# Performance work log

Measured on AMD Instinct MI355X. Metric: run time of the kernel, lower is better.

Reference implementation:

```python
import jax, jax.numpy as jnp
import numpy as np

B, N, D = 2, 2048, 768
HEADS, DIM_HEAD = 12, 64
INNER = HEADS * DIM_HEAD  # 768
OUT_DIM = 768


def setup_inputs() -> dict:
    key = jax.random.key(0)
    k1, k2, k3, k4, k5 = jax.random.split(key, 5)
    s_in = 1.0 / np.sqrt(D)
    s_inner = 1.0 / np.sqrt(INNER)
    return {
        "x": jax.random.normal(k1, (B, N, D), dtype=jnp.float32),
        "w_qkv": jax.random.normal(k2, (D, 3 * INNER), dtype=jnp.float32) * s_in,
        "b_qkv": jax.random.normal(k3, (3 * INNER,), dtype=jnp.float32) * 0.01,
        "w_out": jax.random.normal(k4, (INNER, OUT_DIM), dtype=jnp.float32) * s_inner,
        "b_out": jax.random.normal(k5, (OUT_DIM,), dtype=jnp.float32) * 0.01,
    }


def reference(x, w_qkv, b_qkv, w_out, b_out):
    b, n, _ = x.shape
    scale = DIM_HEAD ** -0.5
    qkv = x @ w_qkv + b_qkv                      # [b, n, 3*inner]
    q, k, v = jnp.split(qkv, 3, axis=-1)
    # 'b n (h d) -> b h n d'
    reshape = lambda t: t.reshape(b, n, HEADS, DIM_HEAD).transpose(0, 2, 1, 3)
    q, k, v = reshape(q), reshape(k), reshape(v)
    dots = jnp.einsum("bhnd,bhmd->bhnm", q, k) * scale
    attn = jax.nn.softmax(dots, axis=-1)
    out = jnp.einsum("bhnm,bhmd->bhnd", attn, v)  # [b, h, n, d]
    out = out.transpose(0, 2, 1, 3).reshape(b, n, INNER)
    return out @ w_out + b_out
```

## Files before the change

### kernel.cpp

```cpp
#include <hip/hip_runtime.h>
#include <hip/hip_bf16.h>
#include <stdint.h>


typedef __attribute__((ext_vector_type(8))) short bf16x8;
typedef __attribute__((ext_vector_type(4))) float f32x4;
typedef __attribute__((address_space(3))) unsigned int lds_uint;
typedef __attribute__((address_space(1))) const unsigned int g_uint;

__device__ __forceinline__ short f2bf(float f) {
    union { float f; uint32_t u; } x; x.f = f;
    uint32_t r = (x.u + 0x7fffu + ((x.u >> 16) & 1u)) >> 16;
    return (short)r;
}
__device__ __forceinline__ uint32_t packbf(float a, float b) {
    union { float f; uint32_t u; } xa, xb; xa.f = a; xb.f = b;
    return __builtin_amdgcn_perm(xb.u + 0x8000u, xa.u + 0x8000u, 0x07060302u);
}
__device__ __forceinline__ float exp2fast(float x) {
#if __has_builtin(__builtin_amdgcn_exp2f)
    return __builtin_amdgcn_exp2f(x);
#else
    return __expf(x * 0.6931471805599453f);
#endif
}
__device__ __forceinline__ void gl_lds16(const void* g, void* l) {
    __builtin_amdgcn_global_load_lds((g_uint*)g, (lds_uint*)l, 16, 0, 0);
}

__device__ __forceinline__ void tr_tile(const float* __restrict__ W,
                                        short* __restrict__ Wt, int K, int N,
                                        int n0, int k0, int t, short* S) {
    {
        int kl = t >> 2, ng = t & 3;
        const float* src = W + (size_t)(k0 + kl) * N + n0 + ng * 16;
        #pragma unroll
        for (int j = 0; j < 16; j += 4) {
            float4 f = *(const float4*)(src + j);
            S[(ng*16 + j + 0) * 65 + kl] = f2bf(f.x);
            S[(ng*16 + j + 1) * 65 + kl] = f2bf(f.y);
            S[(ng*16 + j + 2) * 65 + kl] = f2bf(f.z);
            S[(ng*16 + j + 3) * 65 + kl] = f2bf(f.w);
        }
    }
    __syncthreads();
    {
        int nl = t >> 2, kg = t & 3;
        short* dst = Wt + (size_t)(n0 + nl) * K + k0 + kg * 16;
        #pragma unroll
        for (int j = 0; j < 16; j += 4) {
            short4 s4;
            s4.x = S[nl*65 + kg*16 + j + 0];
            s4.y = S[nl*65 + kg*16 + j + 1];
            s4.z = S[nl*65 + kg*16 + j + 2];
            s4.w = S[nl*65 + kg*16 + j + 3];
            *(short4*)(dst + j) = s4;
        }
    }
}

__global__ __launch_bounds__(256)
void prep_k(const float* __restrict__ x, short* __restrict__ Xb,
            const float* __restrict__ Wq, short* __restrict__ Wqt,
            const float* __restrict__ Wo, short* __restrict__ Wot)
{
    __shared__ short S[64 * 65];
    const int t = threadIdx.x;
    if (blockIdx.x < 1536) {
        int i = (blockIdx.x * 256 + t) * 8;
        float4 f0 = *(const float4*)(x + i);
        float4 f1 = *(const float4*)(x + i + 4);
        short s[8];
        s[0]=f2bf(f0.x); s[1]=f2bf(f0.y); s[2]=f2bf(f0.z); s[3]=f2bf(f0.w);
        s[4]=f2bf(f1.x); s[5]=f2bf(f1.y); s[6]=f2bf(f1.z); s[7]=f2bf(f1.w);
        *(uint4*)(Xb + i) = *(uint4*)s;
        return;
    }
    if (blockIdx.x < 1968) {
        const int b2 = blockIdx.x - 1536;
        tr_tile(Wq, Wqt, 768, 2304, (b2 % 36) * 64, (b2 / 36) * 64, t, S);
    } else {
        const int b3 = blockIdx.x - 1968;
        tr_tile(Wo, Wot, 768, 768, (b3 % 12) * 64, (b3 / 12) * 64, t, S);
    }
}

__global__ __launch_bounds__(256)
void tr_w(const float* __restrict__ W, short* __restrict__ Wt, int K, int N) {
    __shared__ short S[64 * 65];
    tr_tile(W, Wt, K, N, blockIdx.x * 64, blockIdx.y * 64, threadIdx.x, S);
}

__global__ __launch_bounds__(256)
void gemm_qkv(const short* __restrict__ A, const short* __restrict__ Bt,
              const float* __restrict__ bias,
              short* __restrict__ Qb, short* __restrict__ Kb, short* __restrict__ Vt)
{
    __shared__ short As[2][128 * 32];
    __shared__ short Bs[2][96 * 32];
    const int tid = threadIdx.x, lane = tid & 63, w = tid >> 6;
    const int wm = w >> 1, wn = w & 1, quad = lane >> 4, lcol = lane & 15;
    const int bm = blockIdx.y * 128, bn = blockIdx.x * 96;

    f32x4 acc[4][3];
    #pragma unroll
    for (int i = 0; i < 4; i++)
        #pragma unroll
        for (int j = 0; j < 3; j++) acc[i][j] = (f32x4){0.f, 0.f, 0.f, 0.f};

    {
        #pragma unroll
        for (int i = 0; i < 2; i++) {
            int c = tid + i * 256, row = c >> 2, cs = c & 3;
            gl_lds16(A + (size_t)(bm + row) * 768 + cs * 8, As[0] + c * 8);
        }
        int c = tid, row = c >> 2, cs = c & 3;
        gl_lds16(Bt + (size_t)(bn + row) * 768 + cs * 8, Bs[0] + c * 8);
        if (tid < 128) {
            int c2 = 256 + tid, row2 = c2 >> 2, cs2 = c2 & 3;
            gl_lds16(Bt + (size_t)(bn + row2) * 768 + cs2 * 8, Bs[0] + c2 * 8);
        }
    }
    __syncthreads();

    for (int it = 0; it < 24; it++) {
        const int p = it & 1;
        if (it < 23) {
            int kt = (it + 1) * 32;
            #pragma unroll
            for (int i = 0; i < 2; i++) {
                int c = tid + i * 256, row = c >> 2, cs = c & 3;
                gl_lds16(A + (size_t)(bm + row) * 768 + kt + cs * 8, As[p ^ 1] + c * 8);
            }
            int c = tid, row = c >> 2, cs = c & 3;
            gl_lds16(Bt + (size_t)(bn + row) * 768 + kt + cs * 8, Bs[p ^ 1] + c * 8);
            if (tid < 128) {
                int c2 = 256 + tid, row2 = c2 >> 2, cs2 = c2 & 3;
                gl_lds16(Bt + (size_t)(bn + row2) * 768 + kt + cs2 * 8, Bs[p ^ 1] + c2 * 8);
            }
        }
        bf16x8 a[4], b[3];
        #pragma unroll
        for (int tm = 0; tm < 4; tm++)
            a[tm] = *(const bf16x8*)(As[p] + (wm*64 + tm*16 + lcol) * 32 + quad * 8);
        #pragma unroll
        for (int tn = 0; tn < 3; tn++)
            b[tn] = *(const bf16x8*)(Bs[p] + (wn*48 + tn*16 + lcol) * 32 + quad * 8);
        #pragma unroll
        for (int tm = 0; tm < 4; tm++)
            #pragma unroll
            for (int tn = 0; tn < 3; tn++)
                acc[tm][tn] = __builtin_amdgcn_mfma_f32_16x16x32_bf16(a[tm], b[tn], acc[tm][tn], 0, 0, 0);
        __syncthreads();
    }

    const float SCLQ = 0.18033688011112042f;
    #pragma unroll
    for (int tm = 0; tm < 4; tm++) {
        #pragma unroll
        for (int tn = 0; tn < 3; tn++) {
            int col = bn + wn*48 + tn*16 + lcol;
            float bv = bias[col];
            int which = (col >= 1536) ? 2 : (col >= 768 ? 1 : 0);
            int cc = col - which * 768;
            int h = cc >> 6, d = cc & 63;
            int rowbase = bm + wm*64 + tm*16 + quad*4;
            int bb = rowbase >> 11, n0 = rowbase & 2047;
            int bh = bb * 12 + h;
            if (which == 2) {
                short4 s4;
                s4.x = f2bf(acc[tm][tn][0] + bv);
                s4.y = f2bf(acc[tm][tn][1] + bv);
                s4.z = f2bf(acc[tm][tn][2] + bv);
                s4.w = f2bf(acc[tm][tn][3] + bv);
                *(short4*)(Vt + (((size_t)bh*32 + (n0 >> 6))*64 + d)*64 + (n0 & 63)) = s4;
            } else {
                #pragma unroll
                for (int reg = 0; reg < 4; reg++) {
                    float v = acc[tm][tn][reg] + bv;
                    if (which == 0) v *= SCLQ;
                    short* dst = (which == 0) ? Qb : Kb;
                    dst[((size_t)bh*2048 + n0 + reg)*64 + d] = f2bf(v);
                }
            }
        }
    }
}

__global__ __launch_bounds__(256)
void attn_k(const short* __restrict__ Q, const short* __restrict__ K,
            const short* __restrict__ Vt, short* __restrict__ Ab)
{
    __shared__ short Ks[2][4096];
    __shared__ short Vs[2][4096];
    __shared__ short Ps[64 * 72];
    __shared__ float lsum[64];

    const int tid = threadIdx.x, lane = tid & 63, w = tid >> 6;
    const int quad = lane >> 4, lcol = lane & 15;
    const int bid = blockIdx.x;
    const int bh = bid % 24, qt = bid / 24;
    const int b = bh / 12, h = bh - b * 12;

    const short* Kg = K  + (size_t)bh * 131072;
    const short* Vg = Vt + (size_t)bh * 131072;

    bf16x8 qf[4][2];
    {
        const short* Qg = Q + ((size_t)bh * 2048 + (size_t)qt * 64) * 64;
        #pragma unroll
        for (int qs = 0; qs < 4; qs++)
            #pragma unroll
            for (int ks = 0; ks < 2; ks++)
                qf[qs][ks] = *(const bf16x8*)(Qg + (qs*16 + lcol) * 64 + ks*32 + quad*8);
    }

    if (tid < 64) lsum[tid] = 0.f;
    #pragma unroll
    for (int i = 0; i < 2; i++) {
        int c = tid + i * 256, row = c >> 3, cs = c & 7, gc = cs ^ (row & 7);
        gl_lds16(Kg + row * 64 + gc * 8, Ks[0] + c * 8);
        gl_lds16(Vg + row * 64 + gc * 8, Vs[0] + c * 8);
    }
    __syncthreads();

    f32x4 o[4];
    #pragma unroll
    for (int tn = 0; tn < 4; tn++) o[tn] = (f32x4){0.f, 0.f, 0.f, 0.f};
    float lp[4] = {0.f, 0.f, 0.f, 0.f};

    const int krow = w * 16 + lcol;
    const int ksw  = krow & 7;

    for (int kt = 0; kt < 32; kt++) {
        const int p = kt & 1;
        if (kt < 31) {
            #pragma unroll
            for (int i = 0; i < 2; i++) {
                int c = tid + i * 256, row = c >> 3, cs = c & 7, gc = cs ^ (row & 7);
                gl_lds16(Kg + (kt + 1) * 4096 + row * 64 + gc * 8, Ks[p ^ 1] + c * 8);
                gl_lds16(Vg + (kt + 1) * 4096 + row * 64 + gc * 8, Vs[p ^ 1] + c * 8);
            }
        }

        f32x4 st[4];
        #pragma unroll
        for (int qs = 0; qs < 4; qs++) st[qs] = (f32x4){0.f, 0.f, 0.f, 0.f};
        #pragma unroll
        for (int ks = 0; ks < 2; ks++) {
            bf16x8 kf = *(const bf16x8*)(Ks[p] + krow * 64 + (((ks*4 + quad) ^ ksw) << 3));
            #pragma unroll
            for (int qs = 0; qs < 4; qs++)
                st[qs] = __builtin_amdgcn_mfma_f32_16x16x32_bf16(kf, qf[qs][ks], st[qs], 0, 0, 0);
        }

        #pragma unroll
        for (int qs = 0; qs < 4; qs++) {
            float p0 = exp2fast(st[qs][0]), p1 = exp2fast(st[qs][1]);
            float p2 = exp2fast(st[qs][2]), p3 = exp2fast(st[qs][3]);
            lp[qs] += (p0 + p1) + (p2 + p3);
            uint32_t uu[2] = { packbf(p0, p1), packbf(p2, p3) };
            *(uint32_t*)(Ps + (qs*16 + lcol) * 72 + w*16 + quad*4)     = uu[0];
            *(uint32_t*)(Ps + (qs*16 + lcol) * 72 + w*16 + quad*4 + 2) = uu[1];
        }
        __syncthreads();

        #pragma unroll
        for (int ks = 0; ks < 2; ks++) {
            bf16x8 ap = *(const bf16x8*)(Ps + (w*16 + lcol) * 72 + ks * 32 + quad * 8);
            #pragma unroll
            for (int tn = 0; tn < 4; tn++) {
                int row = tn * 16 + lcol;
                bf16x8 bv = *(const bf16x8*)(Vs[p] + row * 64 +
                                             (((ks * 4 + quad) ^ (row & 7)) << 3));
                o[tn] = __builtin_amdgcn_mfma_f32_16x16x32_bf16(ap, bv, o[tn], 0, 0, 0);
            }
        }
        __syncthreads();
    }

    #pragma unroll
    for (int qs = 0; qs < 4; qs++) {
        float v = lp[qs];
        v += __shfl_xor(v, 16, 64);
        v += __shfl_xor(v, 32, 64);
        if (quad == 0) atomicAdd(&lsum[qs*16 + lcol], v);
    }
    __syncthreads();
    #pragma unroll
    for (int tn = 0; tn < 4; tn++) {
        #pragma unroll
        for (int r = 0; r < 4; r++) {
            int q = qt * 64 + w * 16 + quad * 4 + r;
            int d = h * 64 + tn * 16 + lcol;
            float rl = 1.0f / lsum[w * 16 + quad * 4 + r];
            Ab[((size_t)(b * 2048 + q)) * 768 + d] = f2bf(o[tn][r] * rl);
        }
    }
}

__global__ __launch_bounds__(256)
void gemm_out(const short* __restrict__ A, const short* __restrict__ Bt,
              const float* __restrict__ bias, float* __restrict__ Of)
{
    __shared__ short As[2][64 * 32];
    __shared__ short Bs[2][96 * 32];
    const int tid = threadIdx.x, lane = tid & 63, w = tid >> 6;
    const int wm = w >> 1, wn = w & 1, quad = lane >> 4, lcol = lane & 15;
    const int bm = blockIdx.y * 64, bn = blockIdx.x * 96;

    f32x4 acc[2][3];
    #pragma unroll
    for (int i = 0; i < 2; i++)
        #pragma unroll
        for (int j = 0; j < 3; j++) acc[i][j] = (f32x4){0.f, 0.f, 0.f, 0.f};

    {
        int row = tid >> 2, cs = tid & 3;
        gl_lds16(A  + (size_t)(bm + row) * 768 + cs * 8, As[0] + tid * 8);
        gl_lds16(Bt + (size_t)(bn + row) * 768 + cs * 8, Bs[0] + tid * 8);
        if (tid < 128) {
            int c = 256 + tid, row2 = c >> 2, cs2 = c & 3;
            gl_lds16(Bt + (size_t)(bn + row2) * 768 + cs2 * 8, Bs[0] + c * 8);
        }
    }
    __syncthreads();

    for (int it = 0; it < 24; it++) {
        const int p = it & 1;
        if (it < 23) {
            int kt = (it + 1) * 32;
            int row = tid >> 2, cs = tid & 3;
            gl_lds16(A  + (size_t)(bm + row) * 768 + kt + cs * 8, As[p ^ 1] + tid * 8);
            gl_lds16(Bt + (size_t)(bn + row) * 768 + kt + cs * 8, Bs[p ^ 1] + tid * 8);
            if (tid < 128) {
                int c = 256 + tid, row2 = c >> 2, cs2 = c & 3;
                gl_lds16(Bt + (size_t)(bn + row2) * 768 + kt + cs2 * 8, Bs[p ^ 1] + c * 8);
            }
        }
        bf16x8 a[2], b[3];
        #pragma unroll
        for (int tm = 0; tm < 2; tm++)
            a[tm] = *(const bf16x8*)(As[p] + (wm*32 + tm*16 + lcol) * 32 + quad * 8);
        #pragma unroll
        for (int tn = 0; tn < 3; tn++)
            b[tn] = *(const bf16x8*)(Bs[p] + (wn*48 + tn*16 + lcol) * 32 + quad * 8);
        #pragma unroll
        for (int tm = 0; tm < 2; tm++)
            #pragma unroll
            for (int tn = 0; tn < 3; tn++)
                acc[tm][tn] = __builtin_amdgcn_mfma_f32_16x16x32_bf16(a[tm], b[tn], acc[tm][tn], 0, 0, 0);
        __syncthreads();
    }
    #pragma unroll
    for (int tm = 0; tm < 2; tm++) {
        #pragma unroll
        for (int tn = 0; tn < 3; tn++) {
            int col = bn + wn*48 + tn*16 + lcol;
            float bv = bias[col];
            #pragma unroll
            for (int reg = 0; reg < 4; reg++) {
                int row = bm + wm*32 + tm*16 + quad*4 + reg;
                Of[(size_t)row * 768 + col] = acc[tm][tn][reg] + bv;
            }
        }
    }
}

extern "C" void kernel_launch(void* const* d_in, const int* in_sizes, int n_in,
                              void* d_out, int out_size, void* d_ws, size_t ws_size,
                              hipStream_t stream)
{
    (void)in_sizes; (void)n_in; (void)out_size;
    const float* x     = (const float*)d_in[0];
    const float* w_qkv = (const float*)d_in[1];
    const float* b_qkv = (const float*)d_in[2];
    const float* w_out = (const float*)d_in[3];
    const float* b_out = (const float*)d_in[4];
    float* out = (float*)d_out;

    const size_t XSZ = (size_t)4096 * 768;
    const size_t WQ  = (size_t)2304 * 768;
    const size_t WO  = (size_t)768 * 768;
    const size_t HSZ = (size_t)24 * 2048 * 64;
    short* Xb  = (short*)d_ws;
    short* Wqt = Xb + XSZ;
    short* Qb  = Wqt + WQ;
    short* Kb  = Qb + HSZ;
    short* Vt  = Kb + HSZ;
    short* Ab  = Xb;

    const bool sepWot = ws_size >= (XSZ + WQ + 3*HSZ + WO) * sizeof(short);
    short* Wot = sepWot ? (Vt + HSZ) : Wqt;

    if (sepWot) {
        prep_k<<<2112, 256, 0, stream>>>(x, Xb, w_qkv, Wqt, w_out, Wot);
        gemm_qkv<<<dim3(24, 32), 256, 0, stream>>>(Xb, Wqt, b_qkv, Qb, Kb, Vt);
    } else {
        prep_k<<<1968, 256, 0, stream>>>(x, Xb, w_qkv, Wqt, w_out, Wot);
        gemm_qkv<<<dim3(24, 32), 256, 0, stream>>>(Xb, Wqt, b_qkv, Qb, Kb, Vt);
        tr_w<<<dim3(12, 12), 256, 0, stream>>>(w_out, Wot, 768, 768);
    }
    attn_k<<<768, 256, 0, stream>>>(Qb, Kb, Vt, Ab);
    gemm_out<<<dim3(8, 64), 256, 0, stream>>>(Ab, Wot, b_out, out);
}
```

Measured before the change: 165.1 us.

## Keep attention probabilities in registers via permlane swap instead of LDS round-trip

The attention kernel now gives each wave its own 16 query rows across all 64 keys of a tile, instead of 16 keys across all 64 queries. The probabilities from the S=K·Q MFMA are packed to bf16 with v_cvt_pk_bf16_f32 and rearranged in registers with v_permlane16_swap. This replaces the shared-memory P buffer, its mid-loop __syncthreads, and the LDS atomic row-sum reduction with shuffles. The trade-off is more K-fragment LDS reads per wave, a remapped V column index to match the permuted operand layout, and gfx950-specific inline asm.

```diff
diff --git a/kernel.cpp b/kernel.cpp
--- a/kernel.cpp
+++ b/kernel.cpp
@@ -193,8 +193,6 @@
 {
     __shared__ short Ks[2][4096];
     __shared__ short Vs[2][4096];
-    __shared__ short Ps[64 * 72];
-    __shared__ float lsum[64];
 
     const int tid = threadIdx.x, lane = tid & 63, w = tid >> 6;
     const int quad = lane >> 4, lcol = lane & 15;
@@ -205,17 +203,14 @@
     const short* Kg = K  + (size_t)bh * 131072;
     const short* Vg = Vt + (size_t)bh * 131072;
 
-    bf16x8 qf[4][2];
+    bf16x8 qf[2];
     {
         const short* Qg = Q + ((size_t)bh * 2048 + (size_t)qt * 64) * 64;
         #pragma unroll
-        for (int qs = 0; qs < 4; qs++)
-            #pragma unroll
-            for (int ks = 0; ks < 2; ks++)
-                qf[qs][ks] = *(const bf16x8*)(Qg + (qs*16 + lcol) * 64 + ks*32 + quad*8);
-    }
-
-    if (tid < 64) lsum[tid] = 0.f;
+        for (int ks = 0; ks < 2; ks++)
+            qf[ks] = *(const bf16x8*)(Qg + (w*16 + lcol) * 64 + ks*32 + quad*8);
+    }
+
     #pragma unroll
     for (int i = 0; i < 2; i++) {
         int c = tid + i * 256, row = c >> 3, cs = c & 7, gc = cs ^ (row & 7);
@@ -227,10 +222,10 @@
     f32x4 o[4];
     #pragma unroll
     for (int tn = 0; tn < 4; tn++) o[tn] = (f32x4){0.f, 0.f, 0.f, 0.f};
-    float lp[4] = {0.f, 0.f, 0.f, 0.f};
-
-    const int krow = w * 16 + lcol;
-    const int ksw  = krow & 7;
+    float lp = 0.f;
+
+    const int ksw = lcol & 7;
+    const int bq  = ((quad & 1) << 1) | (quad >> 1);
 
     for (int kt = 0; kt < 32; kt++) {
         const int p = kt & 1;
@@ -245,56 +240,66 @@
 
         f32x4 st[4];
         #pragma unroll
-        for (int qs = 0; qs < 4; qs++) st[qs] = (f32x4){0.f, 0.f, 0.f, 0.f};
+        for (int kvs = 0; kvs < 4; kvs++) st[kvs] = (f32x4){0.f, 0.f, 0.f, 0.f};
         #pragma unroll
         for (int ks = 0; ks < 2; ks++) {
-            bf16x8 kf = *(const bf16x8*)(Ks[p] + krow * 64 + (((ks*4 + quad) ^ ksw) << 3));
-            #pragma unroll
-            for (int qs = 0; qs < 4; qs++)
-                st[qs] = __builtin_amdgcn_mfma_f32_16x16x32_bf16(kf, qf[qs][ks], st[qs], 0, 0, 0);
-        }
-
-        #pragma unroll
-        for (int qs = 0; qs < 4; qs++) {
-            float p0 = exp2fast(st[qs][0]), p1 = exp2fast(st[qs][1]);
-            float p2 = exp2fast(st[qs][2]), p3 = exp2fast(st[qs][3]);
-            lp[qs] += (p0 + p1) + (p2 + p3);
-            uint32_t uu[2] = { packbf(p0, p1), packbf(p2, p3) };
-            *(uint32_t*)(Ps + (qs*16 + lcol) * 72 + w*16 + quad*4)     = uu[0];
-            *(uint32_t*)(Ps + (qs*16 + lcol) * 72 + w*16 + quad*4 + 2) = uu[1];
-        }
-        __syncthreads();
-
+            #pragma unroll
+            for (int kvs = 0; kvs < 4; kvs++) {
+                bf16x8 kf = *(const bf16x8*)(Ks[p] + (kvs*16 + lcol) * 64 +
+                                             (((ks*4 + quad) ^ ksw) << 3));
+                st[kvs] = __builtin_amdgcn_mfma_f32_16x16x32_bf16(kf, qf[ks], st[kvs], 0, 0, 0);
+            }
+        }
+
+        uint32_t X[4], Y[4];
+        #pragma unroll
+        for (int kvs = 0; kvs < 4; kvs++) {
+            float p0 = exp2fast(st[kvs][0]), p1 = exp2fast(st[kvs][1]);
+            float p2 = exp2fast(st[kvs][2]), p3 = exp2fast(st[kvs][3]);
+            lp += (p0 + p1) + (p2 + p3);
+            asm("v_cvt_pk_bf16_f32 %0, %1, %2" : "=v"(X[kvs]) : "v"(p0), "v"(p1));
+            asm("v_cvt_pk_bf16_f32 %0, %1, %2" : "=v"(Y[kvs]) : "v"(p2), "v"(p3));
+        }
+
+        bf16x8 pa[2];
         #pragma unroll
         for (int ks = 0; ks < 2; ks++) {
-            bf16x8 ap = *(const bf16x8*)(Ps + (w*16 + lcol) * 72 + ks * 32 + quad * 8);
+            uint32_t a0 = X[2*ks], a1 = X[2*ks + 1];
+            uint32_t b0 = Y[2*ks], b1 = Y[2*ks + 1];
+            asm("v_permlane16_swap_b32 %0, %1" : "+v"(a0), "+v"(a1));
+            asm("v_permlane16_swap_b32 %0, %1" : "+v"(b0), "+v"(b1));
+            union { uint32_t u[4]; bf16x8 v; } pk_;
+            pk_.u[0] = a0; pk_.u[1] = b0; pk_.u[2] = a1; pk_.u[3] = b1;
+            pa[ks] = pk_.v;
+        }
+
+        #pragma unroll
+        for (int ks = 0; ks < 2; ks++) {
             #pragma unroll
             for (int tn = 0; tn < 4; tn++) {
                 int row = tn * 16 + lcol;
                 bf16x8 bv = *(const bf16x8*)(Vs[p] + row * 64 +
-                                             (((ks * 4 + quad) ^ (row & 7)) << 3));
-                o[tn] = __builtin_amdgcn_mfma_f32_16x16x32_bf16(ap, bv, o[tn], 0, 0, 0);
+                                             (((ks*4 + bq) ^ (row & 7)) << 3));
+                o[tn] = __builtin_amdgcn_mfma_f32_16x16x32_bf16(pa[ks], bv, o[tn], 0, 0, 0);
             }
         }
         __syncthreads();
     }
 
-    #pragma unroll
-    for (int qs = 0; qs < 4; qs++) {
-        float v = lp[qs];
-        v += __shfl_xor(v, 16, 64);
-        v += __shfl_xor(v, 32, 64);
-        if (quad == 0) atomicAdd(&lsum[qs*16 + lcol], v);
-    }
-    __syncthreads();
+    lp += __shfl_xor(lp, 16, 64);
+    lp += __shfl_xor(lp, 32, 64);
+    float rl[4];
+    #pragma unroll
+    for (int r = 0; r < 4; r++)
+        rl[r] = 1.0f / __shfl(lp, quad * 4 + r, 64);
+
     #pragma unroll
     for (int tn = 0; tn < 4; tn++) {
         #pragma unroll
         for (int r = 0; r < 4; r++) {
             int q = qt * 64 + w * 16 + quad * 4 + r;
             int d = h * 64 + tn * 16 + lcol;
-            float rl = 1.0f / lsum[w * 16 + quad * 4 + r];
-            Ab[((size_t)(b * 2048 + q)) * 768 + d] = f2bf(o[tn][r] * rl);
+            Ab[((size_t)(b * 2048 + q)) * 768 + d] = f2bf(o[tn][r] * rl[r]);
         }
     }
 }
```

Result: faster. 156.4 us (-5.3%).
